# Optimization experiments

Measured on AMD Instinct MI355X. Metric: run time of the kernel, lower is better.

The kernel has to match this reference:

```python
import jax, jax.numpy as jnp
import numpy as np

NUM_R = 725
NUM_T = 180
EPS = 1e-6


def _hough(img):
    """Discrete Hough transform: params[r, t] = sum of img along line
    x*cos(theta_t) + y*sin(theta_t) = rho_r.
    Gather form: sweep along the longer axis of the line (x-sweep when
    |sin|>=|cos|, else y-sweep) so every line is sampled densely.
    """
    W, H = img.shape  # assume square (W == H) so both sweeps share length
    diag = jnp.sqrt(jnp.asarray(W * W + H * H, dtype=img.dtype))
    thetas = jnp.arange(NUM_T, dtype=img.dtype) * (jnp.pi / NUM_T)      # [T]
    rhos = jnp.linspace(-diag, diag, NUM_R, dtype=img.dtype)            # [R]
    cos_t = jnp.cos(thetas)                                             # [T]
    sin_t = jnp.sin(thetas)                                             # [T]
    n = jnp.arange(W)                                                   # sweep coord [N]
    nf = n.astype(img.dtype)

    rho_b = rhos[:, None, None]          # [R,1,1]
    cos_b = cos_t[None, :, None]         # [1,T,1]
    sin_b = sin_t[None, :, None]
    n_b = nf[None, None, :]              # [1,1,N]

    # --- x-sweep: x = n, y = (rho - x*cos) / sin ---
    sin_safe = jnp.where(jnp.abs(sin_b) < EPS, jnp.asarray(1.0, img.dtype), sin_b)
    y_f = (rho_b - n_b * cos_b) / sin_safe
    y_i = jnp.round(y_f).astype(jnp.int32)                              # [R,T,N]
    valid_x = (y_i >= 0) & (y_i < H)
    vals_x = jnp.where(valid_x,
                       img[n[None, None, :], jnp.clip(y_i, 0, H - 1)],
                       jnp.asarray(0.0, img.dtype))

    # --- y-sweep: y = n, x = (rho - y*sin) / cos ---
    cos_safe = jnp.where(jnp.abs(cos_b) < EPS, jnp.asarray(1.0, img.dtype), cos_b)
    x_f = (rho_b - n_b * sin_b) / cos_safe
    x_i = jnp.round(x_f).astype(jnp.int32)
    valid_y = (x_i >= 0) & (x_i < W)
    vals_y = jnp.where(valid_y,
                       img[jnp.clip(x_i, 0, W - 1), n[None, None, :]],
                       jnp.asarray(0.0, img.dtype))

    use_x = (jnp.abs(sin_t) >= jnp.abs(cos_t))[None, :, None]           # [1,T,1]
    vals = jnp.where(use_x, vals_x, vals_y)
    return jnp.sum(vals, axis=-1)                                        # [R,T]


def setup_inputs() -> dict:
    key = jax.random.key(0)
    img = jax.random.uniform(key, (512, 512), dtype=jnp.float32)
    return {"img": img}


def reference(img):
    return _hough(img)
```

## Files before the change

kernel.cpp:

```cpp
#include <hip/hip_runtime.h>
#include <math.h>

#define W 512
#define H 512
#define NUM_R 725
#define NUM_T 180
#define RCHUNK 64
#define NCHUNK (H / RCHUNK)
#define RPAD 768

#define WS_FLOATS ((size_t)W * H + (size_t)NCHUNK * NUM_T * RPAD)

__global__ __launch_bounds__(256) void transpose_k(const float* __restrict__ in,
                                                   float* __restrict__ out) {
    __shared__ float tile[32][33];
    const int bx = blockIdx.x * 32, by = blockIdx.y * 32;
    const int tx = threadIdx.x, ty = threadIdx.y;
#pragma unroll
    for (int j = 0; j < 32; j += 8)
        tile[ty + j][tx] = in[(size_t)(by + ty + j) * W + (bx + tx)];
    __syncthreads();
#pragma unroll
    for (int j = 0; j < 32; j += 8)
        out[(size_t)(bx + ty + j) * H + (by + tx)] = tile[tx][ty + j];
}

__global__ __launch_bounds__(256) void hough_scatter_k(const float* __restrict__ img,
                                                       const float* __restrict__ imgT,
                                                       float* __restrict__ partial) {
    const int t   = blockIdx.x;
    const int n0  = blockIdx.y * RCHUNK;
    const int tid = threadIdx.x;
    const int wave = tid >> 6;

    __shared__ float racc[4 * RPAD];

    {
        float4* z = (float4*)racc;
#pragma unroll
        for (int k = 0; k < 3; ++k)
            z[tid + 256 * k] = make_float4(0.f, 0.f, 0.f, 0.f);
    }
    __syncthreads();

    const double theta = (double)t * (M_PI / 180.0);
    const double s = sin(theta);
    const double c = cos(theta);
    const bool use_x = fabs(s) >= fabs(c);
    const double diag = sqrt(524288.0);
    const double step = (2.0 * diag) / 724.0;
    const double inv_step = 1.0 / step;

    const double lane_co = (use_x ? s : c) * inv_step;
    const double loop_co = (use_x ? c : s) * inv_step;
    const double dstep   = diag * inv_step;

    const double SC = 4294967296.0;
    const long long laneq = (long long)rint(lane_co * SC);
    const long long lq    = (long long)rint(loop_co * SC);
    const long long lq2   = 2 * lq;
    const long long L1 = laneq, L2 = 2 * laneq, L3 = 3 * laneq;
    const unsigned hwq = (unsigned)(fabs(lane_co) * 0.5 * SC);
    const unsigned A = 0x80000000u - hwq;
    const unsigned B = 2u * hwq;

    const int h  = tid >> 7;
    const int c0 = (tid & 127) * 4;
    const double rowpart = (double)(n0 + h) * loop_co + dstep;
    long long u = (long long)rint((rowpart + (double)c0 * lane_co) * SC) + (1ll << 31);

    float* racc_w = racc + wave * RPAD;
    const float* __restrict__ base = use_x ? img : imgT;
    const float4* rowp = (const float4*)(base + (size_t)(n0 + h) * W) + (tid & 127);

#pragma unroll 4
    for (int j = 0; j < RCHUNK / 2; ++j) {
        const float4 v = rowp[j * (2 * W / 4)];
        const long long u0 = u;
        const long long u1 = u + L1;
        const long long u2 = u + L2;
        const long long u3 = u + L3;
        u += lq2;
        if ((unsigned)u0 - A <= B) racc_w[(int)(u0 >> 32)] += v.x;
        if ((unsigned)u1 - A <= B) racc_w[(int)(u1 >> 32)] += v.y;
        if ((unsigned)u2 - A <= B) racc_w[(int)(u2 >> 32)] += v.z;
        if ((unsigned)u3 - A <= B) racc_w[(int)(u3 >> 32)] += v.w;
    }

    __syncthreads();

    float* dst = partial + ((size_t)blockIdx.y * NUM_T + t) * RPAD;
#pragma unroll
    for (int k = 0; k < 3; ++k) {
        const int r = tid + 256 * k;
        dst[r] = racc[r] + racc[RPAD + r] + racc[2 * RPAD + r] + racc[3 * RPAD + r];
    }
}

__global__ __launch_bounds__(256) void reduce_k(const float* __restrict__ partial,
                                                float* __restrict__ out) {
    const int t = blockIdx.x;
    const int tid = threadIdx.x;
#pragma unroll
    for (int k = 0; k < 3; ++k) {
        const int r = tid + 256 * k;
        if (r < NUM_R) {
            float acc = 0.f;
#pragma unroll
            for (int ch = 0; ch < NCHUNK; ++ch)
                acc += partial[((size_t)ch * NUM_T + t) * RPAD + r];
            out[(size_t)r * NUM_T + t] = acc;
        }
    }
}

__global__ __launch_bounds__(256) void hough_gather_k(const float* __restrict__ img,
                                                      float* __restrict__ out) {
    const int t = blockIdx.x;
    const int r = blockIdx.y * 256 + threadIdx.x;
    const int rc = (r < NUM_R) ? r : (NUM_R - 1);

    const double theta = (double)t * (M_PI / 180.0);
    const double s = sin(theta);
    const double c = cos(theta);
    const bool use_x = fabs(s) >= fabs(c);
    double dd = use_x ? s : c;
    if (fabs(dd) < 1e-6) dd = 1.0;
    const double a = use_x ? c : s;
    const double inv = 1.0 / dd;
    const double nk2 = -(a * inv);
    const double diag = sqrt(524288.0);
    const double step = (2.0 * diag) / 724.0;
    double rho = (double)rc * step - diag;
    if (rc == NUM_R - 1) rho = diag;

    const double SCALE = 1099511627776.0;
    const long long NK2q = (long long)rint(nk2 * SCALE);
    long long Y = (long long)rint(rho * inv * SCALE) + (1ll << 39);

    float acc = 0.f;
    if (use_x) {
#pragma unroll 8
        for (int n = 0; n < W; ++n) {
            const int y = (int)(Y >> 40);
            Y += NK2q;
            const float v = img[n * W + min(max(y, 0), W - 1)];
            acc += ((unsigned)y < (unsigned)W) ? v : 0.f;
        }
    } else {
#pragma unroll 4
        for (int n = 0; n < W; ++n) {
            const int y = (int)(Y >> 40);
            Y += NK2q;
            const float v = img[min(max(y, 0), W - 1) * W + n];
            acc += ((unsigned)y < (unsigned)W) ? v : 0.f;
        }
    }
    if (r < NUM_R) out[(size_t)r * NUM_T + t] = acc;
}

extern "C" void kernel_launch(void* const* d_in, const int* in_sizes, int n_in,
                              void* d_out, int out_size, void* d_ws, size_t ws_size,
                              hipStream_t stream) {
    const float* img = (const float*)d_in[0];
    float* out = (float*)d_out;

    if (ws_size >= WS_FLOATS * sizeof(float)) {
        float* imgT = (float*)d_ws;
        float* partial = (float*)d_ws + (size_t)W * H;

        transpose_k<<<dim3(16, 16), dim3(32, 8), 0, stream>>>(img, imgT);
        hough_scatter_k<<<dim3(NUM_T, NCHUNK), dim3(256), 0, stream>>>(img, imgT, partial);
        reduce_k<<<dim3(NUM_T), dim3(256), 0, stream>>>(partial, out);
    } else {
        hough_gather_k<<<dim3(NUM_T, (NUM_R + 255) / 256), dim3(256), 0, stream>>>(img, out);
    }
}
```

Measured before the change: 81.36 us.

## Fuse partial reduction into scatter kernel via last-block atomic counter

Removes the separate reduce kernel launch. Each scatter block atomically bumps a per-angle counter, and the last block to finish sums the partials for that angle. Counters are zeroed inside the transpose kernel. RCHUNK is halved so there are twice as many blocks (more parallelism), at the cost of more partial buffers to reduce and extra fence/atomic overhead.

```diff
diff --git a/kernel.cpp b/kernel.cpp
--- a/kernel.cpp
+++ b/kernel.cpp
@@ -5,17 +5,24 @@
 #define H 512
 #define NUM_R 725
 #define NUM_T 180
-#define RCHUNK 64
+#define RCHUNK 32
 #define NCHUNK (H / RCHUNK)
 #define RPAD 768
 
-#define WS_FLOATS ((size_t)W * H + (size_t)NCHUNK * NUM_T * RPAD)
+#define WS_IMGT   ((size_t)W * H)
+#define WS_PART   (WS_IMGT + (size_t)NCHUNK * NUM_T * RPAD)
+#define WS_FLOATS (WS_PART + 256)
 
 __global__ __launch_bounds__(256) void transpose_k(const float* __restrict__ in,
-                                                   float* __restrict__ out) {
+                                                   float* __restrict__ out,
+                                                   int* __restrict__ counters) {
     __shared__ float tile[32][33];
     const int bx = blockIdx.x * 32, by = blockIdx.y * 32;
     const int tx = threadIdx.x, ty = threadIdx.y;
+    if (bx == 0 && by == 0) {
+        const int f = ty * 32 + tx;
+        if (f < NUM_T) counters[f] = 0;
+    }
 #pragma unroll
     for (int j = 0; j < 32; j += 8)
         tile[ty + j][tx] = in[(size_t)(by + ty + j) * W + (bx + tx)];
@@ -27,13 +34,16 @@
 
 __global__ __launch_bounds__(256) void hough_scatter_k(const float* __restrict__ img,
                                                        const float* __restrict__ imgT,
-                                                       float* __restrict__ partial) {
+                                                       float* __restrict__ partial,
+                                                       int* __restrict__ counters,
+                                                       float* __restrict__ out) {
     const int t   = blockIdx.x;
     const int n0  = blockIdx.y * RCHUNK;
     const int tid = threadIdx.x;
     const int wave = tid >> 6;
 
     __shared__ float racc[4 * RPAD];
+    __shared__ int isLast;
 
     {
         float4* z = (float4*)racc;
@@ -95,21 +105,25 @@
         const int r = tid + 256 * k;
         dst[r] = racc[r] + racc[RPAD + r] + racc[2 * RPAD + r] + racc[3 * RPAD + r];
     }
-}
+    __syncthreads();
 
-__global__ __launch_bounds__(256) void reduce_k(const float* __restrict__ partial,
-                                                float* __restrict__ out) {
-    const int t = blockIdx.x;
-    const int tid = threadIdx.x;
+    if (tid == 0) {
+        __threadfence();
+        isLast = (atomicAdd(&counters[t], 1) == NCHUNK - 1);
+    }
+    __syncthreads();
+    if (isLast) {
+        __threadfence();
 #pragma unroll
-    for (int k = 0; k < 3; ++k) {
-        const int r = tid + 256 * k;
-        if (r < NUM_R) {
-            float acc = 0.f;
+        for (int k = 0; k < 3; ++k) {
+            const int r = tid + 256 * k;
+            if (r < NUM_R) {
+                float acc = 0.f;
 #pragma unroll
-            for (int ch = 0; ch < NCHUNK; ++ch)
-                acc += partial[((size_t)ch * NUM_T + t) * RPAD + r];
-            out[(size_t)r * NUM_T + t] = acc;
+                for (int ch = 0; ch < NCHUNK; ++ch)
+                    acc += partial[((size_t)ch * NUM_T + t) * RPAD + r];
+                out[(size_t)r * NUM_T + t] = acc;
+            }
         }
     }
 }
@@ -166,12 +180,13 @@
     float* out = (float*)d_out;
 
     if (ws_size >= WS_FLOATS * sizeof(float)) {
-        float* imgT = (float*)d_ws;
-        float* partial = (float*)d_ws + (size_t)W * H;
+        float* imgT    = (float*)d_ws;
+        float* partial = (float*)d_ws + WS_IMGT;
+        int*   counters = (int*)((float*)d_ws + WS_PART);
 
-        transpose_k<<<dim3(16, 16), dim3(32, 8), 0, stream>>>(img, imgT);
-        hough_scatter_k<<<dim3(NUM_T, NCHUNK), dim3(256), 0, stream>>>(img, imgT, partial);
-        reduce_k<<<dim3(NUM_T), dim3(256), 0, stream>>>(partial, out);
+        transpose_k<<<dim3(16, 16), dim3(32, 8), 0, stream>>>(img, imgT, counters);
+        hough_scatter_k<<<dim3(NUM_T, NCHUNK), dim3(256), 0, stream>>>(
+            img, imgT, partial, counters, out);
     } else {
         hough_gather_k<<<dim3(NUM_T, (NUM_R + 255) / 256), dim3(256), 0, stream>>>(img, out);
     }
```

Measured after the change: 179.5 us. +120.7%, slower.
